# Kernel optimization log

Measured on AMD Instinct MI355X. Metric: run time of the kernel, lower is better.

Reference implementation:

```python
import jax, jax.numpy as jnp
import numpy as np

A = 1.0  # slope of hard sigmoid (init arg `a`)


def setup_inputs() -> dict:
    key = jax.random.key(0)
    ks = jax.random.split(key, 10)
    H, B, BOT, TOP = 1024, 4096, 1024, 1024
    stdv = 1.0 / np.sqrt(H)
    u = lambda k, shp: jax.random.uniform(k, shp, jnp.float32, -stdv, stdv)
    U_11 = u(ks[0], (4 * H + 1, H))
    U_21 = u(ks[1], (4 * H + 1, TOP))
    W_01 = u(ks[2], (4 * H + 1, BOT))
    bias = u(ks[3], (4 * H + 1,))
    c = jax.random.normal(ks[4], (H, B), jnp.float32) * 0.1
    h = jnp.tanh(jax.random.normal(ks[5], (H, B), jnp.float32))
    h_bottom = jnp.tanh(jax.random.normal(ks[6], (BOT, B), jnp.float32))
    h_top = jnp.tanh(jax.random.normal(ks[7], (TOP, B), jnp.float32))
    z = (jax.random.uniform(ks[8], (1, B)) > 0.5).astype(jnp.float32)
    z_bottom = (jax.random.uniform(ks[9], (1, B)) > 0.5).astype(jnp.float32)
    return dict(c=c, h_bottom=h_bottom, h=h, h_top=h_top, z=z,
                z_bottom=z_bottom, U_11=U_11, U_21=U_21, W_01=W_01, bias=bias)


def reference(c, h_bottom, h, h_top, z, z_bottom, U_11, U_21, W_01, bias):
    H = U_11.shape[1]
    # [4H+1, B] pre-activations: recurrent + gated top-down + gated bottom-up + bias
    f_s = (W_01 @ h_bottom
           + z * (U_21 @ h_top)
           + z_bottom * (U_11 @ h)
           + bias[:, None])
    f = jax.nn.sigmoid(f_s[0:H])
    i = jax.nn.sigmoid(f_s[H:2 * H])
    o = jax.nn.sigmoid(f_s[2 * H:3 * H])
    g = jnp.tanh(f_s[3 * H:4 * H])
    z_hat = jnp.clip((f_s[4 * H:4 * H + 1] * A + 1.0) / 2.0, 0.0, 1.0)  # hard_sigm
    one = 1.0
    c_new = (z * (i * g)
             + (one - z) * (one - z_bottom) * c
             + (one - z) * z_bottom * (f * c + i * g))
    tanh_c = jnp.tanh(c_new)
    h_new = (z * o * tanh_c
             + (one - z) * (one - z_bottom) * h
             + (one - z) * z_bottom * o * tanh_c)
    # straight-through binary boundary: forward step(z_hat>0.5), backward identity
    z_new = z_hat + jax.lax.stop_gradient((z_hat > 0.5).astype(z_hat.dtype) - z_hat)
    return h_new, c_new, z_new
```

## Files before the change

### kernel.cpp

```cpp
#include <hip/hip_runtime.h>
#include <hip/hip_bf16.h>
#include <math.h>

#define Hd   1024
#define Bsz  4096
#define Kc   3072
#define NT   48

typedef unsigned short u16;
typedef __attribute__((ext_vector_type(8))) u16 u16x8;
typedef __attribute__((ext_vector_type(2))) u16 u16x2;
typedef __attribute__((ext_vector_type(4))) float f32x4;
typedef __attribute__((ext_vector_type(8))) short bf16x8;

__device__ inline u16 f2bf(float f) {
    __hip_bfloat16 h = __float2bfloat16(f);
    return *reinterpret_cast<u16*>(&h);
}

__device__ inline float sigm(float x) { return 1.0f / (1.0f + __expf(-x)); }

__device__ inline void gload16(const void* g, const void* s) {
    __builtin_amdgcn_global_load_lds(
        (const __attribute__((address_space(1))) void*)g,
        (__attribute__((address_space(3))) void*)s, 16, 0, 0);
}

#define BAR()   __builtin_amdgcn_s_barrier()
#define VMW(n)  asm volatile("s_waitcnt vmcnt(" #n ")" ::: "memory")
#define PRIO1() __builtin_amdgcn_s_setprio(1)
#define PRIO0() __builtin_amdgcn_s_setprio(0)

__global__ __launch_bounds__(256) void prep_A(const float* __restrict__ U11,
                                              const float* __restrict__ U21,
                                              const float* __restrict__ W01,
                                              u16* __restrict__ Ab,
                                              float* __restrict__ out) {
    if (blockIdx.x == 0) {
        float* outz = out + (size_t)2 * Hd * Bsz;
        for (int i = threadIdx.x; i < Bsz; i += 256) outz[i] = 0.0f;
    }
    int t = blockIdx.x * 256 + threadIdx.x;
    int row = t / 384;
    int kc = (t - row * 384) * 8;
    int r = row >> 2, gate = row & 3;
    int sel = kc >> 10;
    int k = kc & 1023;
    const float* src = (sel == 0) ? W01 : ((sel == 1) ? U21 : U11);
    const float4* p = reinterpret_cast<const float4*>(src + (size_t)(gate * Hd + r) * Hd + k);
    float4 v0 = p[0], v1 = p[1];
    u16x8 o;
    o[0] = f2bf(v0.x); o[1] = f2bf(v0.y); o[2] = f2bf(v0.z); o[3] = f2bf(v0.w);
    o[4] = f2bf(v1.x); o[5] = f2bf(v1.y); o[6] = f2bf(v1.z); o[7] = f2bf(v1.w);
    *reinterpret_cast<u16x8*>(Ab + (size_t)row * Kc + kc) = o;
}

__global__ __launch_bounds__(256) void prep_B(const float* __restrict__ hb,
                                              const float* __restrict__ ht,
                                              const float* __restrict__ hh,
                                              const float* __restrict__ z,
                                              const float* __restrict__ zb,
                                              const float* __restrict__ U11,
                                              const float* __restrict__ U21,
                                              const float* __restrict__ W01,
                                              u16* __restrict__ Bb,
                                              float* __restrict__ out) {
    __shared__ float tile[64][33];
    __shared__ float red[8][32];
    int n0 = blockIdx.x * 32;
    int kg0 = blockIdx.y * 64;
    int sel = kg0 >> 10;
    int k0 = kg0 & 1023;
    const float* src = (sel == 0) ? hb : ((sel == 1) ? ht : hh);
    const float* wsrc = (sel == 0) ? W01 : ((sel == 1) ? U21 : U11);
    int t = threadIdx.x, tx = t & 31, ty = t >> 5;
#pragma unroll
    for (int j = 0; j < 8; ++j) {
        int kk = ty * 8 + j;
        tile[kk][tx] = src[(size_t)(k0 + kk) * Bsz + n0 + tx];
    }
    __syncthreads();
    {
        int kp = t & 31, ny = t >> 5;
#pragma unroll
        for (int j = 0; j < 4; ++j) {
            int nl = ny * 4 + j;
            int n = n0 + nl;
            float s = (sel == 0) ? 1.0f : ((sel == 1) ? z[n] : zb[n]);
            u16x2 o;
            o[0] = f2bf(tile[kp * 2][nl] * s);
            o[1] = f2bf(tile[kp * 2 + 1][nl] * s);
            *reinterpret_cast<u16x2*>(Bb + (size_t)n * Kc + kg0 + kp * 2) = o;
        }
    }
    {
        int col = t & 31, seg = t >> 5;
        const float* w = wsrc + (size_t)4096 * 1024 + k0 + seg * 8;
        float p = 0.0f;
#pragma unroll
        for (int j = 0; j < 8; ++j) p += w[j] * tile[seg * 8 + j][col];
        red[seg][col] = p;
        __syncthreads();
        if (seg == 0) {
            float tot = 0.0f;
#pragma unroll
            for (int q = 0; q < 8; ++q) tot += red[q][col];
            int n = n0 + col;
            float sca = (sel == 0) ? 1.0f : ((sel == 1) ? z[n] : zb[n]);
            atomicAdd(out + (size_t)2 * Hd * Bsz + n, tot * sca);
        }
    }
}

__global__ __launch_bounds__(512, 2) void gemm_fused(
    const u16* __restrict__ A, const u16* __restrict__ Bm,
    const float* __restrict__ c_in, const float* __restrict__ h_in,
    const float* __restrict__ z, const float* __restrict__ zb,
    const float* __restrict__ bias, float* __restrict__ out) {
    extern __shared__ __align__(16) u16 smem[];
    u16* const AsB = smem;
    u16* const BsB = smem + 32768;

    const int t = threadIdx.x;
    const int w = t >> 6, l = t & 63;
    const int wm = w >> 2, wn = w & 3;

    const int orig = blockIdx.x;
    const int wg = ((orig & 7) << 5) | (orig >> 3);
    const int bm = wg >> 4, bn = wg & 15;

    const int srow = t >> 3;
    const int sgs  = (t & 7) ^ (srow & 7);
    const int fr = l & 15, fq = l >> 4, fkey = l & 7;

    f32x4 acc[8][4];
#pragma unroll
    for (int i = 0; i < 8; ++i)
#pragma unroll
        for (int j = 0; j < 4; ++j) acc[i][j] = (f32x4){0.f, 0.f, 0.f, 0.f};

    const u16* gA = A  + (size_t)(bm * 256 + srow) * Kc + sgs * 8;
    const u16* gB = Bm + (size_t)(bn * 256 + srow) * Kc + sgs * 8;

    auto stageA = [&](int buf, int half, int kt) {
#pragma unroll
        for (int iss = 0; iss < 2; ++iss) {
            const u16* g = gA + (size_t)(half * 128 + iss * 64) * Kc + kt * 64;
            const u16* d = AsB + buf * 16384 + (half * 128 + iss * 64 + (w << 3)) * 64;
            gload16(g, d);
        }
    };
    auto stageB = [&](int buf, int half, int kt) {
#pragma unroll
        for (int iss = 0; iss < 2; ++iss) {
            const u16* g = gB + (size_t)(half * 128 + iss * 64) * Kc + kt * 64;
            const u16* d = BsB + buf * 16384 + (half * 128 + iss * 64 + (w << 3)) * 64;
            gload16(g, d);
        }
    };

    bf16x8 aF[2][4][2];
    bf16x8 bF[2][2][2];

    auto readA = [&](int buf, int mh, int miL, int ks) -> bf16x8 {
        int r = mh * 128 + wm * 64 + miL * 16 + fr;
        int g = ((ks << 2) + fq) ^ fkey;
        return *reinterpret_cast<const bf16x8*>(AsB + buf * 16384 + r * 64 + g * 8);
    };
    auto readB = [&](int buf, int nh, int niL, int ks) -> bf16x8 {
        int r = nh * 128 + wn * 32 + niL * 16 + fr;
        int g = ((ks << 2) + fq) ^ fkey;
        return *reinterpret_cast<const bf16x8*>(BsB + buf * 16384 + r * 64 + g * 8);
    };

#define MFMAQ(mh, nh)                                                         \
    PRIO1();                                                                  \
    _Pragma("unroll")                                                         \
    for (int mi = 0; mi < 4; ++mi)                                            \
        _Pragma("unroll")                                                     \
        for (int ni = 0; ni < 2; ++ni)                                        \
            _Pragma("unroll")                                                 \
            for (int ks = 0; ks < 2; ++ks)                                    \
                acc[(mh)*4 + mi][(nh)*2 + ni] =                               \
                    __builtin_amdgcn_mfma_f32_16x16x32_bf16(                  \
                        aF[mh][mi][ks], bF[nh][ni][ks],                       \
                        acc[(mh)*4 + mi][(nh)*2 + ni], 0, 0, 0);              \
    PRIO0()

    stageA(0, 0, 0); stageB(0, 0, 0); stageA(0, 1, 0); stageB(0, 1, 0);
    VMW(3); BAR();

    for (int T = 0; T < NT; ++T) {
        const int p = T & 1, q2 = p ^ 1;
        const bool more = (T + 1 < NT);
#pragma unroll
        for (int j = 0; j < 4; ++j) {
            aF[0][j][0] = readA(p, 0, j, 0); aF[0][j][1] = readA(p, 0, j, 1);
        }
#pragma unroll
        for (int j = 0; j < 2; ++j) {
            bF[0][j][0] = readB(p, 0, j, 0); bF[0][j][1] = readB(p, 0, j, 1);
        }
        if (more) { stageA(q2, 0, T + 1); VMW(3); } else { VMW(2); }
        BAR();
        MFMAQ(0, 0);
#pragma unroll
        for (int j = 0; j < 4; ++j) {
            aF[1][j][0] = readA(p, 1, j, 0); aF[1][j][1] = readA(p, 1, j, 1);
        }
        if (more) { stageB(q2, 0, T + 1); VMW(3); } else { VMW(0); }
        BAR();
        MFMAQ(1, 0);
#pragma unroll
        for (int j = 0; j < 2; ++j) {
            bF[1][j][0] = readB(p, 1, j, 0); bF[1][j][1] = readB(p, 1, j, 1);
        }
        if (more) { stageA(q2, 1, T + 1); stageB(q2, 1, T + 1); VMW(3); }
        BAR();
        MFMAQ(1, 1);
        MFMAQ(0, 1);
    }

    const int rB = bm * 64;
    const int nB = bn * 256;
    float zc[4], zbv[4];
#pragma unroll
    for (int ni = 0; ni < 4; ++ni) {
        int n = nB + (ni >> 1) * 128 + wn * 32 + (ni & 1) * 16 + fr;
        zc[ni] = z[n]; zbv[ni] = zb[n];
    }
#pragma unroll
    for (int mi = 0; mi < 8; ++mi) {
        const int r = rB + (mi >> 2) * 32 + wm * 16 + (mi & 3) * 4 + fq;
        const float b0 = bias[r], b1 = bias[Hd + r], b2 = bias[2 * Hd + r], b3 = bias[3 * Hd + r];
        const float* crow = c_in + (size_t)r * Bsz;
        const float* hrow = h_in + (size_t)r * Bsz;
        float* hout = out + (size_t)r * Bsz;
        float* cout = out + (size_t)Hd * Bsz + (size_t)r * Bsz;
#pragma unroll
        for (int ni = 0; ni < 4; ++ni) {
            const int n = nB + (ni >> 1) * 128 + wn * 32 + (ni & 1) * 16 + fr;
            f32x4 a = acc[mi][ni];
            float co = crow[n], ho = hrow[n];
            float fg = sigm(a[0] + b0);
            float ig = sigm(a[1] + b1);
            float og = sigm(a[2] + b2);
            float gg = tanhf(a[3] + b3);
            float i_g = ig * gg;
            float nz = 1.0f - zc[ni], nzb = 1.0f - zbv[ni];
            float cn = zc[ni] * i_g + nz * nzb * co + nz * zbv[ni] * (fg * co + i_g);
            float tc2 = tanhf(cn);
            float hn = zc[ni] * og * tc2 + nz * nzb * ho + nz * zbv[ni] * og * tc2;
            hout[n] = hn; cout[n] = cn;
        }
    }

    if (bm == 0 && t < 256) {
        float* outz = out + (size_t)2 * Hd * Bsz;
        int n = bn * 256 + t;
        float s = outz[n] + bias[4096];
        float zh = (s + 1.0f) * 0.5f;
        zh = fminf(fmaxf(zh, 0.0f), 1.0f);
        outz[n] = (zh > 0.5f) ? 1.0f : 0.0f;
    }
#undef MFMAQ
}

extern "C" void kernel_launch(void* const* d_in, const int* in_sizes, int n_in,
                              void* d_out, int out_size, void* d_ws, size_t ws_size,
                              hipStream_t stream) {
    (void)in_sizes; (void)n_in; (void)out_size; (void)ws_size;
    const float* c    = (const float*)d_in[0];
    const float* hb   = (const float*)d_in[1];
    const float* h    = (const float*)d_in[2];
    const float* ht   = (const float*)d_in[3];
    const float* z    = (const float*)d_in[4];
    const float* zb   = (const float*)d_in[5];
    const float* U11  = (const float*)d_in[6];
    const float* U21  = (const float*)d_in[7];
    const float* W01  = (const float*)d_in[8];
    const float* bias = (const float*)d_in[9];
    float* out = (float*)d_out;

    u16* Ab = (u16*)d_ws;
    u16* Bb = Ab + (size_t)4096 * Kc;

    hipFuncSetAttribute(reinterpret_cast<const void*>(gemm_fused),
                        hipFuncAttributeMaxDynamicSharedMemorySize, 131072);

    prep_A<<<6144, 256, 0, stream>>>(U11, U21, W01, Ab, out);
    prep_B<<<dim3(128, 48), 256, 0, stream>>>(hb, ht, h, z, zb, U11, U21, W01, Bb, out);
    gemm_fused<<<256, 512, 131072, stream>>>(Ab, Bb, c, h, z, zb, bias, out);
}
```

Before: 124.3 us.

## Pre-pack operands into MFMA fragment tiles and shrink GEMM block to 256x128

The prep kernels now write A and B in a tiled fragment-major layout (16-row by 32-k chunks), so the GEMM can stream each tile with one contiguous 16-byte load per lane and read fragments from LDS without swizzling. The GEMM drops from a 256x256 tile with 128 KB LDS and a split-phase schedule to a 256x128 tile with 48 KB LDS, a simple double buffer with k-step 32, and 512 blocks at a higher occupancy target. This is meant to cut LDS bank conflicts and address arithmetic and to raise occupancy. The cost is less operand reuse per block, twice as many k-iterations with barriers each time, and more redundant global traffic.

```diff
diff --git a/kernel.cpp b/kernel.cpp
--- a/kernel.cpp
+++ b/kernel.cpp
@@ -5,11 +5,11 @@
 #define Hd   1024
 #define Bsz  4096
 #define Kc   3072
-#define NT   48
+#define NTt  96
+#define CH   512
 
 typedef unsigned short u16;
 typedef __attribute__((ext_vector_type(8))) u16 u16x8;
-typedef __attribute__((ext_vector_type(2))) u16 u16x2;
 typedef __attribute__((ext_vector_type(4))) float f32x4;
 typedef __attribute__((ext_vector_type(8))) short bf16x8;
 
@@ -30,29 +30,42 @@
 #define VMW(n)  asm volatile("s_waitcnt vmcnt(" #n ")" ::: "memory")
 #define PRIO1() __builtin_amdgcn_s_setprio(1)
 #define PRIO0() __builtin_amdgcn_s_setprio(0)
+
 
 __global__ __launch_bounds__(256) void prep_A(const float* __restrict__ U11,
                                               const float* __restrict__ U21,
                                               const float* __restrict__ W01,
                                               u16* __restrict__ Ab,
                                               float* __restrict__ out) {
-    if (blockIdx.x == 0) {
+    __shared__ u16 lds[16 * 520];
+    if (blockIdx.x == 0 && blockIdx.y == 0) {
         float* outz = out + (size_t)2 * Hd * Bsz;
         for (int i = threadIdx.x; i < Bsz; i += 256) outz[i] = 0.0f;
     }
-    int t = blockIdx.x * 256 + threadIdx.x;
-    int row = t / 384;
-    int kc = (t - row * 384) * 8;
-    int r = row >> 2, gate = row & 3;
-    int sel = kc >> 10;
-    int k = kc & 1023;
+    const int mb = blockIdx.x, kb = blockIdx.y;
+    const int t = threadIdx.x;
+    const int r16 = t >> 4, j = t & 15;
+    const int row = mb * 16 + r16, gate = row & 3, r = row >> 2;
+    const int sel = kb >> 1;
+    const int k0 = (kb & 1) * 512 + j * 32;
     const float* src = (sel == 0) ? W01 : ((sel == 1) ? U21 : U11);
-    const float4* p = reinterpret_cast<const float4*>(src + (size_t)(gate * Hd + r) * Hd + k);
-    float4 v0 = p[0], v1 = p[1];
-    u16x8 o;
-    o[0] = f2bf(v0.x); o[1] = f2bf(v0.y); o[2] = f2bf(v0.z); o[3] = f2bf(v0.w);
-    o[4] = f2bf(v1.x); o[5] = f2bf(v1.y); o[6] = f2bf(v1.z); o[7] = f2bf(v1.w);
-    *reinterpret_cast<u16x8*>(Ab + (size_t)row * Kc + kc) = o;
+    const float4* p = reinterpret_cast<const float4*>(
+        src + ((size_t)(gate * Hd + r)) * Hd + k0);
+#pragma unroll
+    for (int g = 0; g < 4; ++g) {
+        float4 v0 = p[g * 2], v1 = p[g * 2 + 1];
+        u16x8 o;
+        o[0] = f2bf(v0.x); o[1] = f2bf(v0.y); o[2] = f2bf(v0.z); o[3] = f2bf(v0.w);
+        o[4] = f2bf(v1.x); o[5] = f2bf(v1.y); o[6] = f2bf(v1.z); o[7] = f2bf(v1.w);
+        *reinterpret_cast<u16x8*>(&lds[j * 520 + (g * 16 + r16) * 8]) = o;
+    }
+    __syncthreads();
+    const int c = t >> 4, jj = t & 15;
+    u16* gdst = Ab + ((size_t)(mb * NTt + kb * 16 + c)) * CH;
+#pragma unroll
+    for (int i = 0; i < 4; ++i)
+        *reinterpret_cast<u16x8*>(gdst + i * 128 + jj * 8) =
+            *reinterpret_cast<const u16x8*>(&lds[c * 520 + i * 128 + jj * 8]);
 }
 
 __global__ __launch_bounds__(256) void prep_B(const float* __restrict__ hb,
@@ -67,13 +80,13 @@
                                               float* __restrict__ out) {
     __shared__ float tile[64][33];
     __shared__ float red[8][32];
-    int n0 = blockIdx.x * 32;
-    int kg0 = blockIdx.y * 64;
-    int sel = kg0 >> 10;
-    int k0 = kg0 & 1023;
+    const int n0 = blockIdx.x * 32;
+    const int kg0 = blockIdx.y * 64;
+    const int sel = kg0 >> 10;
+    const int k0 = kg0 & 1023;
     const float* src = (sel == 0) ? hb : ((sel == 1) ? ht : hh);
     const float* wsrc = (sel == 0) ? W01 : ((sel == 1) ? U21 : U11);
-    int t = threadIdx.x, tx = t & 31, ty = t >> 5;
+    const int t = threadIdx.x, tx = t & 31, ty = t >> 5;
 #pragma unroll
     for (int j = 0; j < 8; ++j) {
         int kk = ty * 8 + j;
@@ -81,17 +94,18 @@
     }
     __syncthreads();
     {
-        int kp = t & 31, ny = t >> 5;
-#pragma unroll
-        for (int j = 0; j < 4; ++j) {
-            int nl = ny * 4 + j;
-            int n = n0 + nl;
-            float s = (sel == 0) ? 1.0f : ((sel == 1) ? z[n] : zb[n]);
-            u16x2 o;
-            o[0] = f2bf(tile[kp * 2][nl] * s);
-            o[1] = f2bf(tile[kp * 2 + 1][nl] * s);
-            *reinterpret_cast<u16x2*>(Bb + (size_t)n * Kc + kg0 + kp * 2) = o;
-        }
+        const int c = t >> 6, l = t & 63, g = l >> 4, n16 = l & 15;
+        const int kt_loc = c & 1, nb_loc = c >> 1;
+        const int nl = nb_loc * 16 + n16;
+        const int n = n0 + nl;
+        const float s = (sel == 0) ? 1.0f : ((sel == 1) ? z[n] : zb[n]);
+        u16x8 o;
+#pragma unroll
+        for (int e = 0; e < 8; ++e)
+            o[e] = f2bf(tile[kt_loc * 32 + g * 8 + e][nl] * s);
+        const int nb = (n0 >> 4) + nb_loc, kt = (kg0 >> 5) + kt_loc;
+        *reinterpret_cast<u16x8*>(Bb + ((size_t)(nb * NTt + kt)) * CH +
+                                  (g * 16 + n16) * 8) = o;
     }
     {
         int col = t & 31, seg = t >> 5;
@@ -112,134 +126,97 @@
     }
 }
 
-__global__ __launch_bounds__(512, 2) void gemm_fused(
+__global__ __launch_bounds__(512, 4) void gemm_fused(
     const u16* __restrict__ A, const u16* __restrict__ Bm,
     const float* __restrict__ c_in, const float* __restrict__ h_in,
     const float* __restrict__ z, const float* __restrict__ zb,
     const float* __restrict__ bias, float* __restrict__ out) {
     extern __shared__ __align__(16) u16 smem[];
-    u16* const AsB = smem;
-    u16* const BsB = smem + 32768;
+    u16* const As = smem;
+    u16* const Bs = smem + 16384;
 
     const int t = threadIdx.x;
     const int w = t >> 6, l = t & 63;
     const int wm = w >> 2, wn = w & 3;
+    const int fr = l & 15, fq = l >> 4;
 
     const int orig = blockIdx.x;
-    const int wg = ((orig & 7) << 5) | (orig >> 3);
-    const int bm = wg >> 4, bn = wg & 15;
-
-    const int srow = t >> 3;
-    const int sgs  = (t & 7) ^ (srow & 7);
-    const int fr = l & 15, fq = l >> 4, fkey = l & 7;
-
-    f32x4 acc[8][4];
+    const int wg = ((orig & 7) << 6) | (orig >> 3);
+    const int bm = wg >> 5, bn = wg & 31;
+
+    f32x4 acc[8][2];
 #pragma unroll
     for (int i = 0; i < 8; ++i)
 #pragma unroll
-        for (int j = 0; j < 4; ++j) acc[i][j] = (f32x4){0.f, 0.f, 0.f, 0.f};
-
-    const u16* gA = A  + (size_t)(bm * 256 + srow) * Kc + sgs * 8;
-    const u16* gB = Bm + (size_t)(bn * 256 + srow) * Kc + sgs * 8;
-
-    auto stageA = [&](int buf, int half, int kt) {
+        for (int j = 0; j < 2; ++j) acc[i][j] = (f32x4){0.f, 0.f, 0.f, 0.f};
+
+    auto stageA = [&](int buf, int kt) {
 #pragma unroll
         for (int iss = 0; iss < 2; ++iss) {
-            const u16* g = gA + (size_t)(half * 128 + iss * 64) * Kc + kt * 64;
-            const u16* d = AsB + buf * 16384 + (half * 128 + iss * 64 + (w << 3)) * 64;
-            gload16(g, d);
+            int mb = bm * 16 + iss * 8 + w;
+            gload16(A + ((size_t)(mb * NTt + kt)) * CH + l * 8,
+                    As + buf * 8192 + iss * 4096 + w * 512 + l * 8);
         }
     };
-    auto stageB = [&](int buf, int half, int kt) {
-#pragma unroll
-        for (int iss = 0; iss < 2; ++iss) {
-            const u16* g = gB + (size_t)(half * 128 + iss * 64) * Kc + kt * 64;
-            const u16* d = BsB + buf * 16384 + (half * 128 + iss * 64 + (w << 3)) * 64;
-            gload16(g, d);
-        }
+    auto stageB = [&](int buf, int kt) {
+        int nb = bn * 8 + w;
+        gload16(Bm + ((size_t)(nb * NTt + kt)) * CH + l * 8,
+                Bs + buf * 4096 + w * 512 + l * 8);
     };
 
-    bf16x8 aF[2][4][2];
-    bf16x8 bF[2][2][2];
-
-    auto readA = [&](int buf, int mh, int miL, int ks) -> bf16x8 {
-        int r = mh * 128 + wm * 64 + miL * 16 + fr;
-        int g = ((ks << 2) + fq) ^ fkey;
-        return *reinterpret_cast<const bf16x8*>(AsB + buf * 16384 + r * 64 + g * 8);
-    };
-    auto readB = [&](int buf, int nh, int niL, int ks) -> bf16x8 {
-        int r = nh * 128 + wn * 32 + niL * 16 + fr;
-        int g = ((ks << 2) + fq) ^ fkey;
-        return *reinterpret_cast<const bf16x8*>(BsB + buf * 16384 + r * 64 + g * 8);
-    };
-
-#define MFMAQ(mh, nh)                                                         \
-    PRIO1();                                                                  \
-    _Pragma("unroll")                                                         \
-    for (int mi = 0; mi < 4; ++mi)                                            \
-        _Pragma("unroll")                                                     \
-        for (int ni = 0; ni < 2; ++ni)                                        \
-            _Pragma("unroll")                                                 \
-            for (int ks = 0; ks < 2; ++ks)                                    \
-                acc[(mh)*4 + mi][(nh)*2 + ni] =                               \
-                    __builtin_amdgcn_mfma_f32_16x16x32_bf16(                  \
-                        aF[mh][mi][ks], bF[nh][ni][ks],                       \
-                        acc[(mh)*4 + mi][(nh)*2 + ni], 0, 0, 0);              \
-    PRIO0()
-
-    stageA(0, 0, 0); stageB(0, 0, 0); stageA(0, 1, 0); stageB(0, 1, 0);
-    VMW(3); BAR();
-
-    for (int T = 0; T < NT; ++T) {
-        const int p = T & 1, q2 = p ^ 1;
-        const bool more = (T + 1 < NT);
-#pragma unroll
-        for (int j = 0; j < 4; ++j) {
-            aF[0][j][0] = readA(p, 0, j, 0); aF[0][j][1] = readA(p, 0, j, 1);
-        }
-#pragma unroll
-        for (int j = 0; j < 2; ++j) {
-            bF[0][j][0] = readB(p, 0, j, 0); bF[0][j][1] = readB(p, 0, j, 1);
-        }
-        if (more) { stageA(q2, 0, T + 1); VMW(3); } else { VMW(2); }
+    stageA(0, 0); stageB(0, 0);
+
+    for (int T = 0; T < NTt; ++T) {
+        const int p = T & 1;
+        if (T + 1 < NTt) {
+            stageA(p ^ 1, T + 1); stageB(p ^ 1, T + 1);
+            VMW(3);
+        } else {
+            VMW(0);
+        }
         BAR();
-        MFMAQ(0, 0);
-#pragma unroll
-        for (int j = 0; j < 4; ++j) {
-            aF[1][j][0] = readA(p, 1, j, 0); aF[1][j][1] = readA(p, 1, j, 1);
-        }
-        if (more) { stageB(q2, 0, T + 1); VMW(3); } else { VMW(0); }
+        const u16* Ap = As + p * 8192;
+        const u16* Bpp = Bs + p * 4096;
+        bf16x8 bF0 = *reinterpret_cast<const bf16x8*>(Bpp + (wn * 2 + 0) * CH + l * 8);
+        bf16x8 bF1 = *reinterpret_cast<const bf16x8*>(Bpp + (wn * 2 + 1) * CH + l * 8);
+        PRIO1();
+#pragma unroll
+        for (int h2 = 0; h2 < 2; ++h2) {
+            bf16x8 a0 = *reinterpret_cast<const bf16x8*>(Ap + (wm * 8 + h2 * 4 + 0) * CH + l * 8);
+            bf16x8 a1 = *reinterpret_cast<const bf16x8*>(Ap + (wm * 8 + h2 * 4 + 1) * CH + l * 8);
+            bf16x8 a2 = *reinterpret_cast<const bf16x8*>(Ap + (wm * 8 + h2 * 4 + 2) * CH + l * 8);
+            bf16x8 a3 = *reinterpret_cast<const bf16x8*>(Ap + (wm * 8 + h2 * 4 + 3) * CH + l * 8);
+            acc[h2 * 4 + 0][0] = __builtin_amdgcn_mfma_f32_16x16x32_bf16(a0, bF0, acc[h2 * 4 + 0][0], 0, 0, 0);
+            acc[h2 * 4 + 0][1] = __builtin_amdgcn_mfma_f32_16x16x32_bf16(a0, bF1, acc[h2 * 4 + 0][1], 0, 0, 0);
+            acc[h2 * 4 + 1][0] = __builtin_amdgcn_mfma_f32_16x16x32_bf16(a1, bF0, acc[h2 * 4 + 1][0], 0, 0, 0);
+            acc[h2 * 4 + 1][1] = __builtin_amdgcn_mfma_f32_16x16x32_bf16(a1, bF1, acc[h2 * 4 + 1][1], 0, 0, 0);
+            acc[h2 * 4 + 2][0] = __builtin_amdgcn_mfma_f32_16x16x32_bf16(a2, bF0, acc[h2 * 4 + 2][0], 0, 0, 0);
+            acc[h2 * 4 + 2][1] = __builtin_amdgcn_mfma_f32_16x16x32_bf16(a2, bF1, acc[h2 * 4 + 2][1], 0, 0, 0);
+            acc[h2 * 4 + 3][0] = __builtin_amdgcn_mfma_f32_16x16x32_bf16(a3, bF0, acc[h2 * 4 + 3][0], 0, 0, 0);
+            acc[h2 * 4 + 3][1] = __builtin_amdgcn_mfma_f32_16x16x32_bf16(a3, bF1, acc[h2 * 4 + 3][1], 0, 0, 0);
+        }
+        PRIO0();
         BAR();
-        MFMAQ(1, 0);
-#pragma unroll
-        for (int j = 0; j < 2; ++j) {
-            bF[1][j][0] = readB(p, 1, j, 0); bF[1][j][1] = readB(p, 1, j, 1);
-        }
-        if (more) { stageA(q2, 1, T + 1); stageB(q2, 1, T + 1); VMW(3); }
-        BAR();
-        MFMAQ(1, 1);
-        MFMAQ(0, 1);
-    }
-
-    const int rB = bm * 64;
-    const int nB = bn * 256;
-    float zc[4], zbv[4];
-#pragma unroll
-    for (int ni = 0; ni < 4; ++ni) {
-        int n = nB + (ni >> 1) * 128 + wn * 32 + (ni & 1) * 16 + fr;
+    }
+
+    float zc[2], zbv[2];
+#pragma unroll
+    for (int ni = 0; ni < 2; ++ni) {
+        int n = bn * 128 + wn * 32 + ni * 16 + fr;
         zc[ni] = z[n]; zbv[ni] = zb[n];
     }
 #pragma unroll
     for (int mi = 0; mi < 8; ++mi) {
-        const int r = rB + (mi >> 2) * 32 + wm * 16 + (mi & 3) * 4 + fq;
-        const float b0 = bias[r], b1 = bias[Hd + r], b2 = bias[2 * Hd + r], b3 = bias[3 * Hd + r];
+        const int r = bm * 64 + wm * 32 + mi * 4 + fq;
+        const float b0 = bias[r], b1 = bias[Hd + r];
+        const float b2 = bias[2 * Hd + r], b3 = bias[3 * Hd + r];
         const float* crow = c_in + (size_t)r * Bsz;
         const float* hrow = h_in + (size_t)r * Bsz;
         float* hout = out + (size_t)r * Bsz;
         float* cout = out + (size_t)Hd * Bsz + (size_t)r * Bsz;
 #pragma unroll
-        for (int ni = 0; ni < 4; ++ni) {
-            const int n = nB + (ni >> 1) * 128 + wn * 32 + (ni & 1) * 16 + fr;
+        for (int ni = 0; ni < 2; ++ni) {
+            const int n = bn * 128 + wn * 32 + ni * 16 + fr;
             f32x4 a = acc[mi][ni];
             float co = crow[n], ho = hrow[n];
             float fg = sigm(a[0] + b0);
@@ -255,15 +232,14 @@
         }
     }
 
-    if (bm == 0 && t < 256) {
+    if (bm == 0 && t < 128) {
         float* outz = out + (size_t)2 * Hd * Bsz;
-        int n = bn * 256 + t;
+        int n = bn * 128 + t;
         float s = outz[n] + bias[4096];
         float zh = (s + 1.0f) * 0.5f;
         zh = fminf(fmaxf(zh, 0.0f), 1.0f);
         outz[n] = (zh > 0.5f) ? 1.0f : 0.0f;
     }
-#undef MFMAQ
 }
 
 extern "C" void kernel_launch(void* const* d_in, const int* in_sizes, int n_in,
@@ -283,12 +259,12 @@
     float* out = (float*)d_out;
 
     u16* Ab = (u16*)d_ws;
-    u16* Bb = Ab + (size_t)4096 * Kc;
+    u16* Bb = Ab + (size_t)256 * NTt * CH;
 
     hipFuncSetAttribute(reinterpret_cast<const void*>(gemm_fused),
-                        hipFuncAttributeMaxDynamicSharedMemorySize, 131072);
-
-    prep_A<<<6144, 256, 0, stream>>>(U11, U21, W01, Ab, out);
+                        hipFuncAttributeMaxDynamicSharedMemorySize, 49152);
+
+    prep_A<<<dim3(256, 6), 256, 0, stream>>>(U11, U21, W01, Ab, out);
     prep_B<<<dim3(128, 48), 256, 0, stream>>>(hb, ht, h, z, zb, U11, U21, W01, Bb, out);
-    gemm_fused<<<256, 512, 131072, stream>>>(Ab, Bb, c, h, z, zb, bias, out);
-}
+    gemm_fused<<<512, 512, 49152, stream>>>(Ab, Bb, c, h, z, zb, bias, out);
+}
```

After: 123.3 us. No clear change (-0.7%).
